# Optimization experiments

Measured on AMD Instinct MI355X. Metric: run time of the kernel, lower is better.

Reference implementation:

```python
import jax, jax.numpy as jnp
import numpy as np

B, S, D, H = 4, 1024, 1024, 16
DH = D // H  # head dim = 64
PAD = -1e7   # padding_num in source
EPS = 1e-3   # keras LayerNormalization default epsilon


def setup_inputs() -> dict:
    key = jax.random.key(0)
    ks = jax.random.split(key, 8)
    return {
        "queries": jax.random.normal(ks[0], (B, S, D), jnp.float32),
        "keys": jax.random.normal(ks[1], (B, S, D), jnp.float32),
        "values": jax.random.normal(ks[2], (B, S, D), jnp.float32),
        "query_masks": jax.random.randint(ks[3], (B, S), 0, 2, jnp.int32),
        "key_masks": jax.random.randint(ks[4], (B, S), 0, 2, jnp.int32),
        "Wq": jax.random.normal(ks[5], (D, D), jnp.float32) * (D ** -0.5),
        "Wk": jax.random.normal(ks[6], (D, D), jnp.float32) * (D ** -0.5),
        "Wv": jax.random.normal(ks[7], (D, D), jnp.float32) * (D ** -0.5),
        "gamma": jnp.ones((D,), jnp.float32),
        "beta": jnp.zeros((D,), jnp.float32),
    }


def reference(queries, keys, values, query_masks, key_masks, Wq, Wk, Wv, gamma, beta):
    # QKV projections (no bias)
    Q = queries @ Wq  # [B,S,D]
    K = keys @ Wk
    V = values @ Wv
    # split heads: tf.split(axis=2)+concat(axis=0) == head-major layout [H,B,S,DH]
    Qh = Q.reshape(B, S, H, DH).transpose(2, 0, 1, 3)
    Kh = K.reshape(B, S, H, DH).transpose(2, 0, 1, 3)
    Vh = V.reshape(B, S, H, DH).transpose(2, 0, 1, 3)
    # scaled scores; note source scales by head_dim ** 0.5 (d_k of split K)
    scores = jnp.einsum("hbqd,hbkd->hbqk", Qh, Kh) / (DH ** 0.5)
    # additive key mask: positions where key_mask==0 get large negative
    scores = jnp.where(key_masks[None, :, None, :] == 0, PAD, scores)
    attn = jax.nn.softmax(scores, axis=-1)
    # multiplicative query mask AFTER softmax (as in source)
    attn = attn * query_masks[None, :, :, None].astype(jnp.float32)
    out = jnp.einsum("hbqk,hbkd->hbqd", attn, Vh)  # [H,B,S,DH]
    # merge heads back: concat over feature axis in head order
    out = out.transpose(1, 2, 0, 3).reshape(B, S, D)
    # residual + LayerNorm
    res = queries + out
    mean = jnp.mean(res, axis=-1, keepdims=True)
    var = jnp.mean(jnp.square(res - mean), axis=-1, keepdims=True)
    return gamma * (res - mean) * jax.lax.rsqrt(var + EPS) + beta
```

## Files before the change

### kernel.cpp

```cpp
#include <hip/hip_runtime.h>

#define BB   4
#define SS   1024
#define DD   1024
#define HH   16
#define DHH  64
#define LN_EPS  (1e-3f)

typedef unsigned short u16;
typedef __attribute__((ext_vector_type(8))) short bf16x8;
typedef __attribute__((ext_vector_type(4))) float f32x4;

__device__ __forceinline__ u16 f2bf(float f) {
    union { float f; unsigned int u; } v; v.f = f;
    return (u16)((v.u + 0x7FFFu + ((v.u >> 16) & 1u)) >> 16);
}

__device__ __forceinline__ unsigned int cvt_pk_bf16(float lo, float hi) {
    unsigned int r;
    asm("v_cvt_pk_bf16_f32 %0, %1, %2" : "=v"(r) : "v"(lo), "v"(hi));
    return r;
}

__device__ __forceinline__ void cp16(void* lds, const void* g) {
    __builtin_amdgcn_global_load_lds(
        (const __attribute__((address_space(1))) unsigned int*)g,
        (__attribute__((address_space(3))) unsigned int*)lds, 16, 0, 0);
}

__global__ __launch_bounds__(256) void prep(const float* __restrict__ q,
                                            const float* __restrict__ k,
                                            const float* __restrict__ v,
                                            const float* __restrict__ Wq,
                                            const float* __restrict__ Wk,
                                            const float* __restrict__ Wv,
                                            u16* __restrict__ Abf,
                                            u16* __restrict__ WtA) {
    __shared__ float Ts[64][65];
    const int z = blockIdx.z;
    const int tid = threadIdx.x;
    if (z < 3) {
        const float* src = (z == 0) ? q : (z == 1) ? k : v;
        u16* dst = Abf + (size_t)z * ((size_t)BB * SS * DD);
        const int N8 = BB * SS * DD / 8;
        for (int i = blockIdx.x * 256 + tid; i < N8; i += 256 * 256) {
            const float4 f0 = ((const float4*)src)[i * 2];
            const float4 f1 = ((const float4*)src)[i * 2 + 1];
            union { u16 u[8]; uint4 o; } t;
            t.u[0] = f2bf(f0.x); t.u[1] = f2bf(f0.y);
            t.u[2] = f2bf(f0.z); t.u[3] = f2bf(f0.w);
            t.u[4] = f2bf(f1.x); t.u[5] = f2bf(f1.y);
            t.u[6] = f2bf(f1.z); t.u[7] = f2bf(f1.w);
            ((uint4*)dst)[i] = t.o;
        }
    } else {
        const float* W = (z == 3) ? Wq : (z == 4) ? Wk : Wv;
        u16* Wt = WtA + (size_t)(z - 3) * DD * DD;
        const int k0 = (blockIdx.x >> 4) * 64, n0 = (blockIdx.x & 15) * 64;
        #pragma unroll
        for (int it = 0; it < 4; ++it) {
            const int idx = tid + it * 256;
            const int r = idx >> 4, c4 = (idx & 15) * 4;
            const float4 vv = *(const float4*)&W[(size_t)(k0 + r) * DD + n0 + c4];
            Ts[r][c4 + 0] = vv.x; Ts[r][c4 + 1] = vv.y;
            Ts[r][c4 + 2] = vv.z; Ts[r][c4 + 3] = vv.w;
        }
        __syncthreads();
        const int n = tid >> 2, kc = (tid & 3) * 16;
        #pragma unroll
        for (int p = 0; p < 8; ++p) {
            const unsigned int lo = f2bf(Ts[kc + p * 2 + 0][n]);
            const unsigned int hi = f2bf(Ts[kc + p * 2 + 1][n]);
            *(unsigned int*)&Wt[(size_t)(n0 + n) * DD + k0 + kc + p * 2] = lo | (hi << 16);
        }
    }
}

__global__ __launch_bounds__(512, 2) void gemm_fused(const u16* __restrict__ Abf,
                                                     const u16* __restrict__ WtA,
                                                     u16* __restrict__ Qbf,
                                                     u16* __restrict__ Kbf,
                                                     u16* __restrict__ Vtb) {
    __shared__ u16 lds[2][2][2][8192];

    const int bid = blockIdx.x;
    const int swz = (bid & 7) * 24 + (bid >> 3);
    const int z   = swz >> 6;
    const int rem = swz & 63;
    const int m0  = (rem >> 2) * 256;
    const int n0  = (rem & 3) * 256;

    const u16* A  = Abf + (size_t)z * ((size_t)BB * SS * DD);
    const u16* Bm = WtA + (size_t)z * (DD * DD);

    const int tid  = threadIdx.x;
    const int wave = tid >> 6, lane = tid & 63;
    const int ln = lane & 15, quad = lane >> 4;
    const int wr = wave >> 2, wc = wave & 3;

    int r_[2], c_[2];
    #pragma unroll
    for (int rd = 0; rd < 2; ++rd) {
        const int l = rd * 512 + tid;
        const int rr = l >> 2, cs = l & 3;
        r_[rd] = rr;
        c_[rd] = cs ^ ((rr >> 1) & 3);
    }
    const u16* srcA[2] = { A  + (size_t)(m0 + r_[0]) * DD + c_[0] * 8,
                           A  + (size_t)(m0 + r_[1]) * DD + c_[1] * 8 };
    const u16* srcB[2] = { Bm + (size_t)(n0 + r_[0]) * DD + c_[0] * 8,
                           Bm + (size_t)(n0 + r_[1]) * DD + c_[1] * 8 };

    int offA[8], offB[4];
    #pragma unroll
    for (int mi = 0; mi < 8; ++mi) {
        const int r = wr * 128 + mi * 16 + ln;
        offA[mi] = (r * 4 + (quad ^ ((r >> 1) & 3))) * 8;
    }
    #pragma unroll
    for (int nj = 0; nj < 4; ++nj) {
        const int r = wc * 64 + nj * 16 + ln;
        offB[nj] = (r * 4 + (quad ^ ((r >> 1) & 3))) * 8;
    }

    auto stage = [&](int T, int x) {
        const int cb = T & 1;
        const int koff = T * 64 + x * 32;
        #pragma unroll
        for (int rd = 0; rd < 2; ++rd) {
            cp16(&lds[cb][x][0][(rd * 512 + wave * 64) * 8], srcA[rd] + koff);
            cp16(&lds[cb][x][1][(rd * 512 + wave * 64) * 8], srcB[rd] + koff);
        }
    };

    f32x4 acc[8][4] = {};

    stage(0, 0); stage(0, 1); stage(1, 0);
    asm volatile("s_waitcnt vmcnt(8)" ::: "memory");
    __builtin_amdgcn_s_barrier();

    #pragma unroll
    for (int t = 0; t < 16; ++t) {
        const int c = t & 1;
        #pragma unroll
        for (int x = 0; x < 2; ++x) {
            if (x == 0) { if (t < 15) stage(t + 1, 1); }
            else        { if (t < 14) stage(t + 2, 0); }

            bf16x8 af[8], bfv[4];
            const u16* Ar = &lds[c][x][0][0];
            const u16* Br = &lds[c][x][1][0];
            #pragma unroll
            for (int mi = 0; mi < 8; ++mi) af[mi] = *(const bf16x8*)&Ar[offA[mi]];
            #pragma unroll
            for (int nj = 0; nj < 4; ++nj) bfv[nj] = *(const bf16x8*)&Br[offB[nj]];

            if (x == 0) {
                if (t < 15) asm volatile("s_waitcnt vmcnt(8)" ::: "memory");
                else        asm volatile("s_waitcnt vmcnt(0)" ::: "memory");
            } else {
                if (t < 14)       asm volatile("s_waitcnt vmcnt(8)" ::: "memory");
                else if (t == 14) asm volatile("s_waitcnt vmcnt(4)" ::: "memory");
            }
            __builtin_amdgcn_s_barrier();

            __builtin_amdgcn_s_setprio(1);
            #pragma unroll
            for (int mi = 0; mi < 8; ++mi)
                #pragma unroll
                for (int nj = 0; nj < 4; ++nj)
                    acc[mi][nj] = __builtin_amdgcn_mfma_f32_16x16x32_bf16(
                        af[mi], bfv[nj], acc[mi][nj], 0, 0, 0);
            __builtin_amdgcn_s_setprio(0);
            __builtin_amdgcn_s_barrier();
        }
    }

    const int hh = (n0 >> 6) + wc;
    if (z < 2) {
        u16* C = (z == 0) ? Qbf : Kbf;
        const float scale = (z == 0) ? 0.18033688f : 1.0f;
        #pragma unroll
        for (int mi = 0; mi < 8; ++mi) {
            const int mbase = m0 + wr * 128 + mi * 16 + quad * 4;
            const int bb = mbase >> 10, sb = mbase & 1023;
            #pragma unroll
            for (int nj = 0; nj < 4; ++nj) {
                const int dh = nj * 16 + ln;
                #pragma unroll
                for (int r = 0; r < 4; ++r)
                    C[(((size_t)bb * HH + hh) * SS + sb + r) * DHH + dh] =
                        f2bf(acc[mi][nj][r] * scale);
            }
        }
    } else {
        #pragma unroll
        for (int mi = 0; mi < 8; ++mi) {
            const int mbase = m0 + wr * 128 + mi * 16 + quad * 4;
            const int bb = mbase >> 10, sb = mbase & 1023;
            #pragma unroll
            for (int nj = 0; nj < 4; ++nj) {
                const int dh = nj * 16 + ln;
                uint2 pk;
                pk.x = cvt_pk_bf16(acc[mi][nj][0], acc[mi][nj][1]);
                pk.y = cvt_pk_bf16(acc[mi][nj][2], acc[mi][nj][3]);
                *(uint2*)&Vtb[(((size_t)bb * HH + hh) * DHH + dh) * SS + sb] = pk;
            }
        }
    }
}

__global__ __launch_bounds__(256) void attn_mfma(const u16* __restrict__ Qg,
                                                 const u16* __restrict__ Kg,
                                                 const u16* __restrict__ Vtg,
                                                 const int* __restrict__ qmask,
                                                 const int* __restrict__ kmask,
                                                 float* __restrict__ O) {
    __shared__ u16 Ps[64 * 68];
    __shared__ u16 Ks[2][64 * 64];
    __shared__ u16 Vs[2][64 * 64];
    __shared__ float kmLds[SS];

    const int bid  = blockIdx.x;
    const int xcd  = bid & 7;
    const int rest = bid >> 3;
    const int bh   = (rest & 7) * 8 + xcd;
    const int qt   = rest >> 3;
    const int b    = bh >> 4, h = bh & 15;
    const int q0   = qt * 64;
    const int tid  = threadIdx.x;
    const int wave = tid >> 6, lane = tid & 63;
    const int ln = lane & 15, quad = lane >> 4;
    const size_t bhs = (size_t)b * HH + h;

    auto stageKV = [&](int t) {
        const int cb = t & 1;
        #pragma unroll
        for (int w = 0; w < 2; ++w) {
            const int s = w * 256 + wave * 64 + lane;
            const int r = s >> 3, csrc = (s & 7) ^ (r & 7);
            cp16(&Ks[cb][(w * 256 + wave * 64) * 8],
                 &Kg[(bhs * SS + t * 64 + r) * DHH + csrc * 8]);
            cp16(&Vs[cb][(w * 256 + wave * 64) * 8],
                 &Vtg[(bhs * DHH + r) * SS + t * 64 + csrc * 8]);
        }
    };

    const u16* qrow = &Qg[(bhs * SS + q0 + wave * 16 + ln) * DHH];
    const bf16x8 qf0 = *(const bf16x8*)&qrow[quad * 8];
    const bf16x8 qf1 = *(const bf16x8*)&qrow[32 + quad * 8];
    asm volatile("" ::: "memory");
    cp16(&kmLds[wave * 256], &kmask[b * SS + (wave * 64 + lane) * 4]);
    stageKV(0);
    stageKV(1);
    asm volatile("s_waitcnt vmcnt(4)" ::: "memory");
    __builtin_amdgcn_s_barrier();

    {
        const int4 iv = *(const int4*)&kmLds[tid * 4];
        float4 fv;
        fv.x = (float)iv.x; fv.y = (float)iv.y;
        fv.z = (float)iv.z; fv.w = (float)iv.w;
        *(float4*)&kmLds[tid * 4] = fv;
    }
    asm volatile("s_waitcnt lgkmcnt(0)" ::: "memory");
    __builtin_amdgcn_s_barrier();

    f32x4 o[4] = {};
    float lsum = 0.f;
    const f32x4 zero = {0.f, 0.f, 0.f, 0.f};
    const int prow = (wave * 16 + ln) * 68;

    #pragma unroll 2
    for (int kt = 0; kt < SS / 64; ++kt) {
        const int cb = kt & 1;
        const u16* Kc = Ks[cb];
        const u16* Vc = Vs[cb];

        #pragma unroll
        for (int nt = 0; nt < 4; ++nt) {
            const int krow = nt * 16 + ln;
            const bf16x8 k0f = *(const bf16x8*)&Kc[((krow << 3) + ((0 + quad) ^ (krow & 7))) << 3];
            const bf16x8 k1f = *(const bf16x8*)&Kc[((krow << 3) + ((4 + quad) ^ (krow & 7))) << 3];
            f32x4 sacc = __builtin_amdgcn_mfma_f32_16x16x32_bf16(k0f, qf0, zero, 0, 0, 0);
            sacc = __builtin_amdgcn_mfma_f32_16x16x32_bf16(k1f, qf1, sacc, 0, 0, 0);
            const float4 fm = *(const float4*)&kmLds[kt * 64 + nt * 16 + quad * 4];
            const float p0 = fm.x * __builtin_amdgcn_exp2f(sacc[0]);
            const float p1 = fm.y * __builtin_amdgcn_exp2f(sacc[1]);
            const float p2 = fm.z * __builtin_amdgcn_exp2f(sacc[2]);
            const float p3 = fm.w * __builtin_amdgcn_exp2f(sacc[3]);
            lsum += (p0 + p1) + (p2 + p3);
            uint2 pk;
            pk.x = cvt_pk_bf16(p0, p1);
            pk.y = cvt_pk_bf16(p2, p3);
            *(uint2*)&Ps[prow + nt * 16 + quad * 4] = pk;
        }

        #pragma unroll
        for (int kk2 = 0; kk2 < 2; ++kk2) {
            const bf16x8 pf = *(const bf16x8*)&Ps[prow + kk2 * 32 + quad * 8];
            #pragma unroll
            for (int nt2 = 0; nt2 < 4; ++nt2) {
                const int vrow = nt2 * 16 + ln;
                const bf16x8 vf = *(const bf16x8*)&Vc[((vrow << 3) + ((kk2 * 4 + quad) ^ (vrow & 7))) << 3];
                o[nt2] = __builtin_amdgcn_mfma_f32_16x16x32_bf16(pf, vf, o[nt2], 0, 0, 0);
            }
        }

        if (kt == SS / 64 - 1) break;
        __builtin_amdgcn_s_barrier();
        if (kt + 2 < SS / 64) {
            stageKV(kt + 2);
            asm volatile("s_waitcnt vmcnt(4)" ::: "memory");
        } else {
            asm volatile("s_waitcnt vmcnt(0)" ::: "memory");
        }
        __builtin_amdgcn_s_barrier();
    }

    lsum += __shfl_xor(lsum, 16);
    lsum += __shfl_xor(lsum, 32);
    #pragma unroll
    for (int r = 0; r < 4; ++r) {
        const int qloc = quad * 4 + r;
        const float l = __shfl(lsum, qloc);
        const int q = q0 + wave * 16 + qloc;
        const float scale = (float)qmask[b * SS + q] / l;
        #pragma unroll
        for (int nt2 = 0; nt2 < 4; ++nt2)
            O[((size_t)b * SS + q) * DD + h * DHH + nt2 * 16 + ln] = o[nt2][r] * scale;
    }
}

__global__ __launch_bounds__(256) void ln_kernel(const float* __restrict__ Qin,
                                                 const float* __restrict__ attn,
                                                 const float* __restrict__ gamma,
                                                 const float* __restrict__ beta,
                                                 float* __restrict__ out) {
    const int row = blockIdx.x;
    const int tid = threadIdx.x;
    const int wid = tid >> 6, lane = tid & 63;
    __shared__ float sred[4];

    const float4 qv = ((const float4*)Qin)[(size_t)row * 256 + tid];
    const float4 av = ((const float4*)attn)[(size_t)row * 256 + tid];
    float4 v;
    v.x = qv.x + av.x; v.y = qv.y + av.y;
    v.z = qv.z + av.z; v.w = qv.w + av.w;

    float sum = v.x + v.y + v.z + v.w;
    #pragma unroll
    for (int off = 32; off; off >>= 1) sum += __shfl_down(sum, off);
    if (lane == 0) sred[wid] = sum;
    __syncthreads();
    const float mean = (sred[0] + sred[1] + sred[2] + sred[3]) * (1.0f / DD);
    __syncthreads();

    const float dx = v.x - mean, dy = v.y - mean, dz = v.z - mean, dw = v.w - mean;
    float vs = dx * dx + dy * dy + dz * dz + dw * dw;
    #pragma unroll
    for (int off = 32; off; off >>= 1) vs += __shfl_down(vs, off);
    if (lane == 0) sred[wid] = vs;
    __syncthreads();
    const float var = (sred[0] + sred[1] + sred[2] + sred[3]) * (1.0f / DD);
    const float inv = rsqrtf(var + LN_EPS);

    const float4 g = ((const float4*)gamma)[tid];
    const float4 bt = ((const float4*)beta)[tid];
    float4 ov;
    ov.x = g.x * dx * inv + bt.x; ov.y = g.y * dy * inv + bt.y;
    ov.z = g.z * dz * inv + bt.z; ov.w = g.w * dw * inv + bt.w;
    ((float4*)out)[(size_t)row * 256 + tid] = ov;
}

extern "C" void kernel_launch(void* const* d_in, const int* in_sizes, int n_in,
                              void* d_out, int out_size, void* d_ws, size_t ws_size,
                              hipStream_t stream) {
    const float* queries = (const float*)d_in[0];
    const float* keys    = (const float*)d_in[1];
    const float* values  = (const float*)d_in[2];
    const int*   qmask   = (const int*)d_in[3];
    const int*   kmask   = (const int*)d_in[4];
    const float* Wq      = (const float*)d_in[5];
    const float* Wk      = (const float*)d_in[6];
    const float* Wv      = (const float*)d_in[7];
    const float* gamma   = (const float*)d_in[8];
    const float* beta    = (const float*)d_in[9];
    float* out = (float*)d_out;

    const size_t NTOK = (size_t)BB * SS;
    u16* Abf = (u16*)d_ws;
    float* Ob = (float*)d_ws;
    u16* Qbf = Abf + 3 * NTOK * DD;
    u16* Kbf = Qbf + NTOK * DD;
    u16* Vtb = Kbf + NTOK * DD;
    u16* WtA = Vtb + NTOK * DD;

    prep<<<dim3(256, 1, 6), 256, 0, stream>>>(queries, keys, values, Wq, Wk, Wv, Abf, WtA);

    gemm_fused<<<192, 512, 0, stream>>>(Abf, WtA, Qbf, Kbf, Vtb);

    attn_mfma<<<BB * HH * (SS / 64), 256, 0, stream>>>(Qbf, Kbf, Vtb, qmask, kmask, Ob);

    ln_kernel<<<BB * SS, 256, 0, stream>>>(queries, Ob, gamma, beta, out);
}
```

Baseline: 199.0 us.

## Double attention query tile to 128 rows with 8 waves sharing K/V stages

```diff
diff --git a/kernel.cpp b/kernel.cpp
--- a/kernel.cpp
+++ b/kernel.cpp
@@ -210,13 +210,13 @@
     }
 }
 
-__global__ __launch_bounds__(256) void attn_mfma(const u16* __restrict__ Qg,
+__global__ __launch_bounds__(512) void attn_mfma(const u16* __restrict__ Qg,
                                                  const u16* __restrict__ Kg,
                                                  const u16* __restrict__ Vtg,
                                                  const int* __restrict__ qmask,
                                                  const int* __restrict__ kmask,
                                                  float* __restrict__ O) {
-    __shared__ u16 Ps[64 * 68];
+    __shared__ u16 Ps[128 * 68];
     __shared__ u16 Ks[2][64 * 64];
     __shared__ u16 Vs[2][64 * 64];
     __shared__ float kmLds[SS];
@@ -227,44 +227,47 @@
     const int bh   = (rest & 7) * 8 + xcd;
     const int qt   = rest >> 3;
     const int b    = bh >> 4, h = bh & 15;
-    const int q0   = qt * 64;
+    const int q0   = qt * 128;
     const int tid  = threadIdx.x;
     const int wave = tid >> 6, lane = tid & 63;
     const int ln = lane & 15, quad = lane >> 4;
     const size_t bhs = (size_t)b * HH + h;
 
+    const int sr = tid >> 3, scsrc = (tid & 7) ^ ((tid >> 3) & 7);
+    const u16* kSrc = &Kg[(bhs * SS + sr) * DHH + scsrc * 8];
+    const u16* vSrc = &Vtg[(bhs * DHH + sr) * SS + scsrc * 8];
     auto stageKV = [&](int t) {
         const int cb = t & 1;
-        #pragma unroll
-        for (int w = 0; w < 2; ++w) {
-            const int s = w * 256 + wave * 64 + lane;
-            const int r = s >> 3, csrc = (s & 7) ^ (r & 7);
-            cp16(&Ks[cb][(w * 256 + wave * 64) * 8],
-                 &Kg[(bhs * SS + t * 64 + r) * DHH + csrc * 8]);
-            cp16(&Vs[cb][(w * 256 + wave * 64) * 8],
-                 &Vtg[(bhs * DHH + r) * SS + t * 64 + csrc * 8]);
-        }
+        cp16(&Ks[cb][wave * 512], kSrc + (size_t)t * 64 * DHH);
+        cp16(&Vs[cb][wave * 512], vSrc + t * 64);
     };
 
     const u16* qrow = &Qg[(bhs * SS + q0 + wave * 16 + ln) * DHH];
     const bf16x8 qf0 = *(const bf16x8*)&qrow[quad * 8];
     const bf16x8 qf1 = *(const bf16x8*)&qrow[32 + quad * 8];
     asm volatile("" ::: "memory");
-    cp16(&kmLds[wave * 256], &kmask[b * SS + (wave * 64 + lane) * 4]);
+    if (wave < 4)
+        cp16(&kmLds[wave * 256], &kmask[b * SS + (wave * 64 + lane) * 4]);
     stageKV(0);
     stageKV(1);
-    asm volatile("s_waitcnt vmcnt(4)" ::: "memory");
+    asm volatile("s_waitcnt vmcnt(2)" ::: "memory");
     __builtin_amdgcn_s_barrier();
 
     {
-        const int4 iv = *(const int4*)&kmLds[tid * 4];
-        float4 fv;
-        fv.x = (float)iv.x; fv.y = (float)iv.y;
-        fv.z = (float)iv.z; fv.w = (float)iv.w;
-        *(float4*)&kmLds[tid * 4] = fv;
+        const int2 iv = *(const int2*)&kmLds[tid * 2];
+        float2 fv; fv.x = (float)iv.x; fv.y = (float)iv.y;
+        *(float2*)&kmLds[tid * 2] = fv;
     }
     asm volatile("s_waitcnt lgkmcnt(0)" ::: "memory");
     __builtin_amdgcn_s_barrier();
+
+    int off[4][2];
+    #pragma unroll
+    for (int nt = 0; nt < 4; ++nt) {
+        const int r = nt * 16 + ln;
+        off[nt][0] = ((r << 3) + ((0 + quad) ^ (r & 7))) << 3;
+        off[nt][1] = ((r << 3) + ((4 + quad) ^ (r & 7))) << 3;
+    }
 
     f32x4 o[4] = {};
     float lsum = 0.f;
@@ -279,9 +282,8 @@
 
         #pragma unroll
         for (int nt = 0; nt < 4; ++nt) {
-            const int krow = nt * 16 + ln;
-            const bf16x8 k0f = *(const bf16x8*)&Kc[((krow << 3) + ((0 + quad) ^ (krow & 7))) << 3];
-            const bf16x8 k1f = *(const bf16x8*)&Kc[((krow << 3) + ((4 + quad) ^ (krow & 7))) << 3];
+            const bf16x8 k0f = *(const bf16x8*)&Kc[off[nt][0]];
+            const bf16x8 k1f = *(const bf16x8*)&Kc[off[nt][1]];
             f32x4 sacc = __builtin_amdgcn_mfma_f32_16x16x32_bf16(k0f, qf0, zero, 0, 0, 0);
             sacc = __builtin_amdgcn_mfma_f32_16x16x32_bf16(k1f, qf1, sacc, 0, 0, 0);
             const float4 fm = *(const float4*)&kmLds[kt * 64 + nt * 16 + quad * 4];
@@ -296,22 +298,23 @@
             *(uint2*)&Ps[prow + nt * 16 + quad * 4] = pk;
         }
 
+        __builtin_amdgcn_s_setprio(1);
         #pragma unroll
         for (int kk2 = 0; kk2 < 2; ++kk2) {
             const bf16x8 pf = *(const bf16x8*)&Ps[prow + kk2 * 32 + quad * 8];
             #pragma unroll
             for (int nt2 = 0; nt2 < 4; ++nt2) {
-                const int vrow = nt2 * 16 + ln;
-                const bf16x8 vf = *(const bf16x8*)&Vc[((vrow << 3) + ((kk2 * 4 + quad) ^ (vrow & 7))) << 3];
+                const bf16x8 vf = *(const bf16x8*)&Vc[off[nt2][kk2]];
                 o[nt2] = __builtin_amdgcn_mfma_f32_16x16x32_bf16(pf, vf, o[nt2], 0, 0, 0);
             }
         }
+        __builtin_amdgcn_s_setprio(0);
 
         if (kt == SS / 64 - 1) break;
         __builtin_amdgcn_s_barrier();
         if (kt + 2 < SS / 64) {
             stageKV(kt + 2);
-            asm volatile("s_waitcnt vmcnt(4)" ::: "memory");
+            asm volatile("s_waitcnt vmcnt(2)" ::: "memory");
         } else {
             asm volatile("s_waitcnt vmcnt(0)" ::: "memory");
         }
@@ -400,7 +403,7 @@
 
     gemm_fused<<<192, 512, 0, stream>>>(Abf, WtA, Qbf, Kbf, Vtb);
 
-    attn_mfma<<<BB * HH * (SS / 64), 256, 0, stream>>>(Qbf, Kbf, Vtb, qmask, kmask, Ob);
+    attn_mfma<<<BB * HH * (SS / 128), 512, 0, stream>>>(Qbf, Kbf, Vtb, qmask, kmask, Ob);
 
     ln_kernel<<<BB * SS, 256, 0, stream>>>(queries, Ob, gamma, beta, out);
 }
```

Result: faster. 186.9 us (-6.1%).
